# Kernel tuning notes

Hardware: AMD Instinct MI355X
Metric: run time of the kernel (lower is better)

Reference implementation:

```python
import jax, jax.numpy as jnp
import numpy as np

N = 200000
F_IN = 165
H = 128
E = 3200000


def gcn_conv(x, edge_index, W, b):
    # x: [N, Fin], edge_index: [2, E], W: [Fin, Fout], b: [Fout]
    n = x.shape[0]
    h = x @ W  # linear transform first (PyG GCNConv)
    # add self loops
    loops = jnp.arange(n, dtype=edge_index.dtype)
    src = jnp.concatenate([edge_index[0], loops])
    dst = jnp.concatenate([edge_index[1], loops])
    # symmetric normalization: deg computed on dst (in-degree incl. self loops)
    deg = jax.ops.segment_sum(jnp.ones_like(dst, dtype=h.dtype), dst, num_segments=n)
    dinv = jnp.where(deg > 0, jax.lax.rsqrt(deg), 0.0)
    norm = dinv[src] * dinv[dst]  # [E+N]
    msgs = h[src] * norm[:, None]  # gather + scale
    out = jax.ops.segment_sum(msgs, dst, num_segments=n)  # scatter-add
    return out + b


def setup_inputs() -> dict:
    key = jax.random.key(0)
    k = jax.random.split(key, 8)
    x = jax.random.normal(k[0], (N, F_IN), dtype=jnp.float32)
    edge_index = jax.random.randint(k[1], (2, E), 0, N, dtype=jnp.int64)
    s1 = 1.0 / np.sqrt(F_IN)
    s2 = 1.0 / np.sqrt(H)
    W1 = jax.random.uniform(k[2], (F_IN, H), jnp.float32, -s1, s1)
    b1 = jnp.zeros((H,), jnp.float32)
    W2 = jax.random.uniform(k[3], (H, H), jnp.float32, -s2, s2)
    b2 = jnp.zeros((H,), jnp.float32)
    Wl = jax.random.uniform(k[4], (H, 2), jnp.float32, -s2, s2)
    bl = jax.random.uniform(k[5], (2,), jnp.float32, -s2, s2)
    return {"x": x, "edge_index": edge_index, "W1": W1, "b1": b1,
            "W2": W2, "b2": b2, "Wl": Wl, "bl": bl}


def reference(x, edge_index, W1, b1, W2, b2, Wl, bl):
    h = gcn_conv(x, edge_index, W1, b1)
    h = jax.nn.relu(h)
    # dropout p=0.3 is identity in eval mode
    h = gcn_conv(h, edge_index, W2, b2)
    h = jax.nn.relu(h)
    return h @ Wl + bl  # [N, 2]
```

## Files before the change

### kernel.cpp

```cpp
#include <hip/hip_runtime.h>
#include <hip/hip_bf16.h>

#define FIN 165
#define HID 128
#define NPB 256
#define MAXNB 784
#define CAP 4608
#define EPB 2048
#define K32C1 6
#define K32C2 4

typedef __attribute__((ext_vector_type(8))) short short8;
typedef __attribute__((ext_vector_type(4))) float float4v;

__device__ inline unsigned bf16rne(float v) {
    unsigned u = __float_as_uint(v);
    return (u + 0x7fffu + ((u >> 16) & 1u)) >> 16;
}

__device__ inline void bf16split(float v, short& h, short& l) {
    unsigned u = __float_as_uint(v);
    unsigned r = u + 0x7fffu + ((u >> 16) & 1u);
    h = (short)(r >> 16);
    float hf = __uint_as_float(((unsigned)(unsigned short)h) << 16);
    float lf = v - hf;
    unsigned u2 = __float_as_uint(lf);
    unsigned r2 = u2 + 0x7fffu + ((u2 >> 16) & 1u);
    l = (short)(r2 >> 16);
}

__device__ inline void bf2_unpack(unsigned u, float& f0, float& f1) {
    f0 = __uint_as_float(u << 16);
    f1 = __uint_as_float(u & 0xffff0000u);
}

__device__ inline void wswz_body(const float* W, short8* out, int K, int k32, int idx) {
    int tot = k32 * 8 * 64;
    if (idx >= tot) return;
    int lane = idx & 63;
    int ct = (idx >> 6) & 7;
    int ks = idx >> 9;
    int col = ct * 16 + (lane & 15);
    int kb = ks * 32 + (lane >> 4) * 8;
    short8 hi, lo;
#pragma unroll
    for (int j = 0; j < 8; ++j) {
        int k = kb + j;
        float v = (k < K) ? W[k * HID + col] : 0.f;
        short h, l;
        bf16split(v, h, l);
        hi[j] = h; lo[j] = l;
    }
    out[idx] = hi;
    out[tot + idx] = lo;
}

__global__ __launch_bounds__(256) void wswz_both(const float* __restrict__ W1p,
                                                 short8* __restrict__ o1,
                                                 const float* __restrict__ W2p,
                                                 short8* __restrict__ o2) {
    int bid = blockIdx.x;
    if (bid < 12) wswz_body(W1p, o1, FIN, K32C1, bid * 256 + threadIdx.x);
    else          wswz_body(W2p, o2, HID, K32C2, (bid - 12) * 256 + threadIdx.x);
}

__global__ __launch_bounds__(256) void bucket_scatter(const int* __restrict__ src,
                                                      const int* __restrict__ dst,
                                                      int* __restrict__ gcur,
                                                      unsigned* __restrict__ bucketed,
                                                      int E, int n, int NB) {
    __shared__ int hist[MAXNB];
    __shared__ int base[MAXNB];
    __shared__ int lcur[MAXNB];
    int tid = threadIdx.x;
    long e0 = (long)blockIdx.x * EPB;
    for (int b = tid; b < NB; b += 256) { hist[b] = 0; lcur[b] = 0; }
    __syncthreads();
    int sv[EPB / 256], dv[EPB / 256];
#pragma unroll
    for (int i = 0; i < EPB / 256; ++i) {
        long e = e0 + i * 256 + tid;
        sv[i] = (e < E) ? src[e] : -1;
        dv[i] = (e < E) ? dst[e] : -1;
        if ((unsigned)dv[i] < (unsigned)n && (unsigned)sv[i] < (unsigned)n)
            atomicAdd(&hist[dv[i] >> 8], 1);
    }
    __syncthreads();
    for (int b = tid; b < NB; b += 256) {
        int h = hist[b];
        base[b] = h ? atomicAdd(&gcur[b * 16], h) : 0;
    }
    __syncthreads();
#pragma unroll
    for (int i = 0; i < EPB / 256; ++i) {
        int d = dv[i], s = sv[i];
        if ((unsigned)d < (unsigned)n && (unsigned)s < (unsigned)n) {
            int bk = d >> 8;
            int idx = base[bk] + atomicAdd(&lcur[bk], 1);
            if ((unsigned)idx < (unsigned)CAP)
                bucketed[(size_t)bk * CAP + idx] =
                    (unsigned)s | ((unsigned)(d & 255) << 18);
        }
    }
}

__global__ __launch_bounds__(256) void bucket_scan(const int* __restrict__ gcur,
                                                   int* __restrict__ bb, int NB,
                                                   int* __restrict__ rowptr, int n) {
    __shared__ int part[256];
    int t = threadIdx.x;
    int v[4];
    int s = 0;
#pragma unroll
    for (int i = 0; i < 4; ++i) {
        int b = t * 4 + i;
        v[i] = (b < NB) ? gcur[b * 16] : 0;
        s += v[i];
    }
    part[t] = s;
    __syncthreads();
    for (int off = 1; off < 256; off <<= 1) {
        int x = (t >= off) ? part[t - off] : 0;
        __syncthreads();
        part[t] += x;
        __syncthreads();
    }
    int run = part[t] - s;
#pragma unroll
    for (int i = 0; i < 4; ++i) {
        int b = t * 4 + i;
        if (b < NB) bb[b] = run;
        run += v[i];
    }
    if (t == 255) { bb[NB] = run; rowptr[n] = run; }
}

__global__ __launch_bounds__(256) void build_csr(const unsigned* __restrict__ bucketed,
                                                 const int* __restrict__ bb,
                                                 float* __restrict__ dinv,
                                                 int* __restrict__ rowptr,
                                                 int* __restrict__ col, int n) {
    __shared__ int deg[NPB];
    __shared__ int scn[NPB];
    __shared__ int cur[NPB];
    int b = blockIdx.x, tid = threadIdx.x;
    int nb0 = b * NPB;
    int ebase = bb[b], cnt = bb[b + 1] - bb[b];
    deg[tid] = 0;
    __syncthreads();
    const unsigned* ep = bucketed + (size_t)b * CAP;
    for (int i = tid; i < cnt; i += 256) {
        unsigned v = ep[i];
        atomicAdd(&deg[(v >> 18) & 255], 1);
    }
    __syncthreads();
    int d = deg[tid];
    scn[tid] = d;
    __syncthreads();
    for (int off = 1; off < 256; off <<= 1) {
        int v = (tid >= off) ? scn[tid - off] : 0;
        __syncthreads();
        scn[tid] += v;
        __syncthreads();
    }
    int excl = scn[tid] - d;
    int node = nb0 + tid;
    if (node < n) {
        dinv[node] = rsqrtf((float)(d + 1));
        rowptr[node] = ebase + excl;
    }
    cur[tid] = excl;
    __syncthreads();
    for (int i = tid; i < cnt; i += 256) {
        unsigned v = ep[i];
        int p = atomicAdd(&cur[(v >> 18) & 255], 1);
        col[ebase + p] = (int)(v & 0x3FFFFu);
    }
}

template <int K32, bool LO_IN_LDS>
__global__ __launch_bounds__(256) void gemm_lds(const float* __restrict__ X,
                                                const short8* __restrict__ Wsw,
                                                const float* __restrict__ dinv,
                                                unsigned* __restrict__ H2,
                                                int K, int kfull, int ntiles) {
    __shared__ short8 sh_hi[K32 * 8 * 64];
    __shared__ short8 sh_lo[LO_IN_LDS ? K32 * 8 * 64 : 1];
    const int tot = K32 * 8 * 64;
    int tid = threadIdx.x;
    for (int i = tid; i < tot; i += 256) sh_hi[i] = Wsw[i];
    if (LO_IN_LDS)
        for (int i = tid; i < tot; i += 256) sh_lo[i] = Wsw[tot + i];
    __syncthreads();
    const short8* wlo_g = Wsw + tot;

    int wave = tid >> 6, lane = tid & 63;
    int m = lane & 15, kph = lane >> 4;

    for (int t = blockIdx.x; t < ntiles; t += gridDim.x) {
        int r0 = t * 64 + wave * 16;
        int row = r0 + m;
        const float* xrow = X + (size_t)row * K + kph * 8;

        float4v acc[8];
#pragma unroll
        for (int ct = 0; ct < 8; ++ct) acc[ct] = (float4v){0.f, 0.f, 0.f, 0.f};

        for (int ks = 0; ks < kfull; ++ks) {
            float xv[8];
#pragma unroll
            for (int j = 0; j < 8; ++j) xv[j] = xrow[ks * 32 + j];
            short8 ah, al;
#pragma unroll
            for (int j = 0; j < 8; ++j) {
                short h, l; bf16split(xv[j], h, l);
                ah[j] = h; al[j] = l;
            }
#pragma unroll
            for (int ct = 0; ct < 8; ++ct) {
                short8 bh = sh_hi[(ks * 8 + ct) * 64 + lane];
                short8 bl = LO_IN_LDS ? sh_lo[(ks * 8 + ct) * 64 + lane]
                                      : wlo_g[(ks * 8 + ct) * 64 + lane];
                acc[ct] = __builtin_amdgcn_mfma_f32_16x16x32_bf16(ah, bh, acc[ct], 0, 0, 0);
                acc[ct] = __builtin_amdgcn_mfma_f32_16x16x32_bf16(al, bh, acc[ct], 0, 0, 0);
                acc[ct] = __builtin_amdgcn_mfma_f32_16x16x32_bf16(ah, bl, acc[ct], 0, 0, 0);
            }
        }
        if (kfull < K32) {
            int ks = kfull;
            int kb = ks * 32 + kph * 8;
            float xv[8];
#pragma unroll
            for (int j = 0; j < 8; ++j) xv[j] = (kb + j < K) ? xrow[ks * 32 + j] : 0.f;
            short8 ah, al;
#pragma unroll
            for (int j = 0; j < 8; ++j) {
                short h, l; bf16split(xv[j], h, l);
                ah[j] = h; al[j] = l;
            }
#pragma unroll
            for (int ct = 0; ct < 8; ++ct) {
                short8 bh = sh_hi[(ks * 8 + ct) * 64 + lane];
                short8 bl = LO_IN_LDS ? sh_lo[(ks * 8 + ct) * 64 + lane]
                                      : wlo_g[(ks * 8 + ct) * 64 + lane];
                acc[ct] = __builtin_amdgcn_mfma_f32_16x16x32_bf16(ah, bh, acc[ct], 0, 0, 0);
                acc[ct] = __builtin_amdgcn_mfma_f32_16x16x32_bf16(al, bh, acc[ct], 0, 0, 0);
                acc[ct] = __builtin_amdgcn_mfma_f32_16x16x32_bf16(ah, bl, acc[ct], 0, 0, 0);
            }
        }
        int ccol = lane & 15, crow = (lane >> 4) * 4;
        bool evenl = (ccol & 1) == 0;
#pragma unroll
        for (int r = 0; r < 4; ++r) {
            int gr = r0 + crow + r;
            float s = dinv[gr];
#pragma unroll
            for (int ct = 0; ct < 8; ++ct) {
                float v = acc[ct][r] * s;
                float p = __shfl_xor(v, 1);
                if (evenl) {
                    unsigned u = bf16rne(v) | (bf16rne(p) << 16);
                    H2[(size_t)gr * 64 + ct * 8 + (ccol >> 1)] = u;
                }
            }
        }
    }
}

__global__ __launch_bounds__(256) void agg_relu(const unsigned* __restrict__ HS2,
                                                const int* __restrict__ rowptr,
                                                const int* __restrict__ col,
                                                const float* __restrict__ dinv,
                                                const float* __restrict__ bias,
                                                float* __restrict__ Y, int n) {
    int lane = threadIdx.x & 63;
    int node = __builtin_amdgcn_readfirstlane(blockIdx.x * 4 + (threadIdx.x >> 6));
    if (node >= n) return;
    int start = __builtin_amdgcn_readfirstlane(rowptr[node]);
    int end   = __builtin_amdgcn_readfirstlane(rowptr[node + 1]);
    float2 acc;
    {
        float f0, f1;
        bf2_unpack(HS2[(size_t)node * 64 + lane], f0, f1);
        acc.x = f0; acc.y = f1;
    }
    int j = start;
    for (; j + 16 <= end; j += 16) {
        unsigned uv[16];
#pragma unroll
        for (int q = 0; q < 16; ++q) {
            int c = col[j + q];
            uv[q] = HS2[(size_t)c * 64 + lane];
        }
#pragma unroll
        for (int q = 0; q < 16; ++q) {
            float f0, f1; bf2_unpack(uv[q], f0, f1);
            acc.x += f0; acc.y += f1;
        }
    }
    while (j < end) {
        unsigned uv[8];
#pragma unroll
        for (int q = 0; q < 8; ++q) {
            int jq = j + q;
            int c = (jq < end) ? col[jq] : node;
            uv[q] = HS2[(size_t)c * 64 + lane];
        }
#pragma unroll
        for (int q = 0; q < 8; ++q) {
            unsigned u = (j + q < end) ? uv[q] : 0u;
            float f0, f1; bf2_unpack(u, f0, f1);
            acc.x += f0; acc.y += f1;
        }
        j += 8;
    }
    float s = dinv[node];
    float2 b = *(const float2*)&bias[2 * lane];
    float2 o;
    o.x = fmaxf(acc.x * s + b.x, 0.f);
    o.y = fmaxf(acc.y * s + b.y, 0.f);
    *(float2*)&Y[(long)node * HID + 2 * lane] = o;
}

__global__ __launch_bounds__(256) void agg_relu_head(const unsigned* __restrict__ HS2,
                                                     const int* __restrict__ rowptr,
                                                     const int* __restrict__ col,
                                                     const float* __restrict__ dinv,
                                                     const float* __restrict__ bias,
                                                     const float* __restrict__ Wl,
                                                     const float* __restrict__ bl,
                                                     float* __restrict__ out, int n) {
    int lane = threadIdx.x & 63;
    int node = __builtin_amdgcn_readfirstlane(blockIdx.x * 4 + (threadIdx.x >> 6));
    if (node >= n) return;
    int start = __builtin_amdgcn_readfirstlane(rowptr[node]);
    int end   = __builtin_amdgcn_readfirstlane(rowptr[node + 1]);
    float2 acc;
    {
        float f0, f1;
        bf2_unpack(HS2[(size_t)node * 64 + lane], f0, f1);
        acc.x = f0; acc.y = f1;
    }
    int j = start;
    for (; j + 16 <= end; j += 16) {
        unsigned uv[16];
#pragma unroll
        for (int q = 0; q < 16; ++q) {
            int c = col[j + q];
            uv[q] = HS2[(size_t)c * 64 + lane];
        }
#pragma unroll
        for (int q = 0; q < 16; ++q) {
            float f0, f1; bf2_unpack(uv[q], f0, f1);
            acc.x += f0; acc.y += f1;
        }
    }
    while (j < end) {
        unsigned uv[8];
#pragma unroll
        for (int q = 0; q < 8; ++q) {
            int jq = j + q;
            int c = (jq < end) ? col[jq] : node;
            uv[q] = HS2[(size_t)c * 64 + lane];
        }
#pragma unroll
        for (int q = 0; q < 8; ++q) {
            unsigned u = (j + q < end) ? uv[q] : 0u;
            float f0, f1; bf2_unpack(u, f0, f1);
            acc.x += f0; acc.y += f1;
        }
        j += 8;
    }
    float s = dinv[node];
    float2 b = *(const float2*)&bias[2 * lane];
    float vx = fmaxf(acc.x * s + b.x, 0.f);
    float vy = fmaxf(acc.y * s + b.y, 0.f);
    float4 wl = *(const float4*)&Wl[4 * lane];
    float a0 = vx * wl.x + vy * wl.z;
    float a1 = vx * wl.y + vy * wl.w;
#pragma unroll
    for (int off = 32; off > 0; off >>= 1) {
        a0 += __shfl_xor(a0, off);
        a1 += __shfl_xor(a1, off);
    }
    if (lane == 0) {
        out[(long)node * 2 + 0] = a0 + bl[0];
        out[(long)node * 2 + 1] = a1 + bl[1];
    }
}

extern "C" void kernel_launch(void* const* d_in, const int* in_sizes, int n_in,
                              void* d_out, int out_size, void* d_ws, size_t ws_size,
                              hipStream_t stream) {
    const float* x  = (const float*)d_in[0];
    const int*   ei = (const int*)d_in[1];
    const float* W1 = (const float*)d_in[2];
    const float* b1 = (const float*)d_in[3];
    const float* W2 = (const float*)d_in[4];
    const float* b2 = (const float*)d_in[5];
    const float* Wl = (const float*)d_in[6];
    const float* bl = (const float*)d_in[7];
    float* out = (float*)d_out;

    int n = in_sizes[0] / FIN;
    int E = in_sizes[1] / 2;
    int NB = (n + NPB - 1) / NPB;
    int ntiles = n / 64;
    const int* srcp = ei;
    const int* dstp = ei + E;

    char* w = (char*)d_ws;
    auto alloc = [&](size_t bytes) {
        char* p = w;
        w += (bytes + 255) & ~(size_t)255;
        return (void*)p;
    };
    int*      gcur    = (int*)     alloc((size_t)NB * 16 * 4);
    int*      bb      = (int*)     alloc(((size_t)NB + 1) * 4);
    int*      rowptr  = (int*)     alloc(((size_t)n + 1) * 4);
    float*    dinv    = (float*)   alloc((size_t)n * 4);
    int*      colv    = (int*)     alloc((size_t)E * 4);
    unsigned* hbuf    = (unsigned*)alloc((size_t)n * 64 * 4);
    float*    ybuf    = (float*)   alloc((size_t)n * HID * 4);
    short8*   w1sw    = (short8*)  alloc((size_t)2 * K32C1 * 8 * 64 * 16);
    short8*   w2sw    = (short8*)  alloc((size_t)2 * K32C2 * 8 * 64 * 16);
    unsigned* bucketed = (unsigned*)ybuf;

    hipMemsetAsync(gcur, 0, (size_t)NB * 16 * 4, stream);

    wswz_both<<<20, 256, 0, stream>>>(W1, w1sw, W2, w2sw);

    bucket_scatter<<<(E + EPB - 1) / EPB, 256, 0, stream>>>(srcp, dstp, gcur,
                                                            bucketed, E, n, NB);
    bucket_scan<<<1, 256, 0, stream>>>(gcur, bb, NB, rowptr, n);
    build_csr<<<NB, 256, 0, stream>>>(bucketed, bb, dinv, rowptr, colv, n);

    gemm_lds<K32C1, false><<<768, 256, 0, stream>>>(x, w1sw, dinv, hbuf,
                                                    FIN, FIN / 32, ntiles);
    agg_relu<<<(n + 3) / 4, 256, 0, stream>>>(hbuf, rowptr, colv, dinv, b1, ybuf, n);

    gemm_lds<K32C2, true><<<512, 256, 0, stream>>>(ybuf, w2sw, dinv, hbuf,
                                                   HID, HID / 32, ntiles);

    agg_relu_head<<<(n + 3) / 4, 256, 0, stream>>>(hbuf, rowptr, colv, dinv, b2,
                                                   Wl, bl, out, n);
}
```

Before: 674.4 us.

## Replace bucketed CSR build with global atomic degree count and direct col fill

```diff
diff --git a/kernel.cpp b/kernel.cpp
--- a/kernel.cpp
+++ b/kernel.cpp
@@ -5,8 +5,6 @@
 #define HID 128
 #define NPB 256
 #define MAXNB 784
-#define CAP 4608
-#define EPB 2048
 #define K32C1 6
 #define K32C2 4
 
@@ -64,49 +62,37 @@
     else          wswz_body(W2p, o2, HID, K32C2, (bid - 12) * 256 + threadIdx.x);
 }
 
-__global__ __launch_bounds__(256) void bucket_scatter(const int* __restrict__ src,
-                                                      const int* __restrict__ dst,
-                                                      int* __restrict__ gcur,
-                                                      unsigned* __restrict__ bucketed,
-                                                      int E, int n, int NB) {
-    __shared__ int hist[MAXNB];
-    __shared__ int base[MAXNB];
-    __shared__ int lcur[MAXNB];
-    int tid = threadIdx.x;
-    long e0 = (long)blockIdx.x * EPB;
-    for (int b = tid; b < NB; b += 256) { hist[b] = 0; lcur[b] = 0; }
+
+__global__ __launch_bounds__(256) void deg_count(const int* __restrict__ dst,
+                                                 int* __restrict__ deg, int E, int n) {
+    int idx = blockIdx.x * 1024 + threadIdx.x;
+#pragma unroll
+    for (int i = 0; i < 4; ++i) {
+        int e = idx + i * 256;
+        if (e < E) {
+            int d = dst[e];
+            if ((unsigned)d < (unsigned)n) atomicAdd(&deg[d], 1);
+        }
+    }
+}
+
+__global__ __launch_bounds__(256) void bsum_reduce(const int* __restrict__ deg,
+                                                   int* __restrict__ bsum, int n) {
+    __shared__ int sm[256];
+    int t = threadIdx.x;
+    int node = blockIdx.x * 256 + t;
+    sm[t] = (node < n) ? deg[node] : 0;
     __syncthreads();
-    int sv[EPB / 256], dv[EPB / 256];
-#pragma unroll
-    for (int i = 0; i < EPB / 256; ++i) {
-        long e = e0 + i * 256 + tid;
-        sv[i] = (e < E) ? src[e] : -1;
-        dv[i] = (e < E) ? dst[e] : -1;
-        if ((unsigned)dv[i] < (unsigned)n && (unsigned)sv[i] < (unsigned)n)
-            atomicAdd(&hist[dv[i] >> 8], 1);
-    }
-    __syncthreads();
-    for (int b = tid; b < NB; b += 256) {
-        int h = hist[b];
-        base[b] = h ? atomicAdd(&gcur[b * 16], h) : 0;
-    }
-    __syncthreads();
-#pragma unroll
-    for (int i = 0; i < EPB / 256; ++i) {
-        int d = dv[i], s = sv[i];
-        if ((unsigned)d < (unsigned)n && (unsigned)s < (unsigned)n) {
-            int bk = d >> 8;
-            int idx = base[bk] + atomicAdd(&lcur[bk], 1);
-            if ((unsigned)idx < (unsigned)CAP)
-                bucketed[(size_t)bk * CAP + idx] =
-                    (unsigned)s | ((unsigned)(d & 255) << 18);
-        }
-    }
-}
-
-__global__ __launch_bounds__(256) void bucket_scan(const int* __restrict__ gcur,
-                                                   int* __restrict__ bb, int NB,
-                                                   int* __restrict__ rowptr, int n) {
+    for (int off = 128; off > 0; off >>= 1) {
+        if (t < off) sm[t] += sm[t + off];
+        __syncthreads();
+    }
+    if (t == 0) bsum[blockIdx.x] = sm[0];
+}
+
+__global__ __launch_bounds__(256) void bscan(const int* __restrict__ bsum,
+                                             int* __restrict__ bb, int NB,
+                                             int* __restrict__ rowptr, int n) {
     __shared__ int part[256];
     int t = threadIdx.x;
     int v[4];
@@ -114,7 +100,7 @@
 #pragma unroll
     for (int i = 0; i < 4; ++i) {
         int b = t * 4 + i;
-        v[i] = (b < NB) ? gcur[b * 16] : 0;
+        v[i] = (b < NB) ? bsum[b] : 0;
         s += v[i];
     }
     part[t] = s;
@@ -132,58 +118,59 @@
         if (b < NB) bb[b] = run;
         run += v[i];
     }
-    if (t == 255) { bb[NB] = run; rowptr[n] = run; }
-}
-
-__global__ __launch_bounds__(256) void build_csr(const unsigned* __restrict__ bucketed,
-                                                 const int* __restrict__ bb,
-                                                 float* __restrict__ dinv,
-                                                 int* __restrict__ rowptr,
-                                                 int* __restrict__ col, int n) {
-    __shared__ int deg[NPB];
-    __shared__ int scn[NPB];
-    __shared__ int cur[NPB];
-    int b = blockIdx.x, tid = threadIdx.x;
-    int nb0 = b * NPB;
-    int ebase = bb[b], cnt = bb[b + 1] - bb[b];
-    deg[tid] = 0;
-    __syncthreads();
-    const unsigned* ep = bucketed + (size_t)b * CAP;
-    for (int i = tid; i < cnt; i += 256) {
-        unsigned v = ep[i];
-        atomicAdd(&deg[(v >> 18) & 255], 1);
-    }
-    __syncthreads();
-    int d = deg[tid];
-    scn[tid] = d;
+    if (t == 255) rowptr[n] = run;
+}
+
+__global__ __launch_bounds__(256) void rowptr_fill(const int* __restrict__ deg,
+                                                   const int* __restrict__ bb,
+                                                   float* __restrict__ dinv,
+                                                   int* __restrict__ rowptr,
+                                                   int* __restrict__ cur, int n) {
+    __shared__ int scn[256];
+    int t = threadIdx.x;
+    int node = blockIdx.x * 256 + t;
+    int d = (node < n) ? deg[node] : 0;
+    scn[t] = d;
     __syncthreads();
     for (int off = 1; off < 256; off <<= 1) {
-        int v = (tid >= off) ? scn[tid - off] : 0;
+        int v = (t >= off) ? scn[t - off] : 0;
         __syncthreads();
-        scn[tid] += v;
+        scn[t] += v;
         __syncthreads();
     }
-    int excl = scn[tid] - d;
-    int node = nb0 + tid;
+    int excl = scn[t] - d;
     if (node < n) {
+        int rp = bb[blockIdx.x] + excl;
+        rowptr[node] = rp;
+        cur[node] = rp;
         dinv[node] = rsqrtf((float)(d + 1));
-        rowptr[node] = ebase + excl;
-    }
-    cur[tid] = excl;
-    __syncthreads();
-    for (int i = tid; i < cnt; i += 256) {
-        unsigned v = ep[i];
-        int p = atomicAdd(&cur[(v >> 18) & 255], 1);
-        col[ebase + p] = (int)(v & 0x3FFFFu);
-    }
-}
-
-template <int K32, bool LO_IN_LDS>
+    }
+}
+
+__global__ __launch_bounds__(256) void col_fill(const int* __restrict__ src,
+                                                const int* __restrict__ dst,
+                                                int* __restrict__ cur,
+                                                int* __restrict__ col, int E, int n) {
+    int idx = blockIdx.x * 1024 + threadIdx.x;
+#pragma unroll
+    for (int i = 0; i < 4; ++i) {
+        int e = idx + i * 256;
+        if (e < E) {
+            int s = src[e], d = dst[e];
+            if ((unsigned)d < (unsigned)n && (unsigned)s < (unsigned)n) {
+                int p = atomicAdd(&cur[d], 1);
+                col[p] = s;
+            }
+        }
+    }
+}
+
+template <int K32, int KFULL, bool LO_IN_LDS>
 __global__ __launch_bounds__(256) void gemm_lds(const float* __restrict__ X,
                                                 const short8* __restrict__ Wsw,
                                                 const float* __restrict__ dinv,
                                                 unsigned* __restrict__ H2,
-                                                int K, int kfull, int ntiles) {
+                                                int K, int ntiles) {
     __shared__ short8 sh_hi[K32 * 8 * 64];
     __shared__ short8 sh_lo[LO_IN_LDS ? K32 * 8 * 64 : 1];
     const int tot = K32 * 8 * 64;
@@ -206,7 +193,8 @@
 #pragma unroll
         for (int ct = 0; ct < 8; ++ct) acc[ct] = (float4v){0.f, 0.f, 0.f, 0.f};
 
-        for (int ks = 0; ks < kfull; ++ks) {
+#pragma unroll
+        for (int ks = 0; ks < KFULL; ++ks) {
             float xv[8];
 #pragma unroll
             for (int j = 0; j < 8; ++j) xv[j] = xrow[ks * 32 + j];
@@ -226,8 +214,8 @@
                 acc[ct] = __builtin_amdgcn_mfma_f32_16x16x32_bf16(ah, bl, acc[ct], 0, 0, 0);
             }
         }
-        if (kfull < K32) {
-            int ks = kfull;
+        if constexpr (KFULL < K32) {
+            const int ks = KFULL;
             int kb = ks * 32 + kph * 8;
             float xv[8];
 #pragma unroll
@@ -415,32 +403,34 @@
         w += (bytes + 255) & ~(size_t)255;
         return (void*)p;
     };
-    int*      gcur    = (int*)     alloc((size_t)NB * 16 * 4);
+    int*      deg     = (int*)     alloc((size_t)n * 4);
+    int*      bsum    = (int*)     alloc((size_t)NB * 4);
     int*      bb      = (int*)     alloc(((size_t)NB + 1) * 4);
     int*      rowptr  = (int*)     alloc(((size_t)n + 1) * 4);
+    int*      cur     = (int*)     alloc((size_t)n * 4);
     float*    dinv    = (float*)   alloc((size_t)n * 4);
     int*      colv    = (int*)     alloc((size_t)E * 4);
     unsigned* hbuf    = (unsigned*)alloc((size_t)n * 64 * 4);
     float*    ybuf    = (float*)   alloc((size_t)n * HID * 4);
     short8*   w1sw    = (short8*)  alloc((size_t)2 * K32C1 * 8 * 64 * 16);
     short8*   w2sw    = (short8*)  alloc((size_t)2 * K32C2 * 8 * 64 * 16);
-    unsigned* bucketed = (unsigned*)ybuf;
-
-    hipMemsetAsync(gcur, 0, (size_t)NB * 16 * 4, stream);
+
+    hipMemsetAsync(deg, 0, (size_t)n * 4, stream);
 
     wswz_both<<<20, 256, 0, stream>>>(W1, w1sw, W2, w2sw);
 
-    bucket_scatter<<<(E + EPB - 1) / EPB, 256, 0, stream>>>(srcp, dstp, gcur,
-                                                            bucketed, E, n, NB);
-    bucket_scan<<<1, 256, 0, stream>>>(gcur, bb, NB, rowptr, n);
-    build_csr<<<NB, 256, 0, stream>>>(bucketed, bb, dinv, rowptr, colv, n);
-
-    gemm_lds<K32C1, false><<<768, 256, 0, stream>>>(x, w1sw, dinv, hbuf,
-                                                    FIN, FIN / 32, ntiles);
+    deg_count<<<(E + 1023) / 1024, 256, 0, stream>>>(dstp, deg, E, n);
+    bsum_reduce<<<NB, 256, 0, stream>>>(deg, bsum, n);
+    bscan<<<1, 256, 0, stream>>>(bsum, bb, NB, rowptr, n);
+    rowptr_fill<<<NB, 256, 0, stream>>>(deg, bb, dinv, rowptr, cur, n);
+    col_fill<<<(E + 1023) / 1024, 256, 0, stream>>>(srcp, dstp, cur, colv, E, n);
+
+    gemm_lds<K32C1, 5, false><<<768, 256, 0, stream>>>(x, w1sw, dinv, hbuf,
+                                                       FIN, ntiles);
     agg_relu<<<(n + 3) / 4, 256, 0, stream>>>(hbuf, rowptr, colv, dinv, b1, ybuf, n);
 
-    gemm_lds<K32C2, true><<<512, 256, 0, stream>>>(ybuf, w2sw, dinv, hbuf,
-                                                   HID, HID / 32, ntiles);
+    gemm_lds<K32C2, 4, true><<<512, 256, 0, stream>>>(ybuf, w2sw, dinv, hbuf,
+                                                      HID, ntiles);
 
     agg_relu_head<<<(n + 3) / 4, 256, 0, stream>>>(hbuf, rowptr, colv, dinv, b2,
                                                    Wl, bl, out, n);
```

New measurement: 996.1 us. 1.48x slower.
